# Kernel tuning notes

Measured on AMD Instinct MI355X. Metric: run time of the kernel, lower is better.

## Reference

```python
import jax, jax.numpy as jnp
import numpy as np

B, NQ, NKV = 2, 2048, 2048
DIM, CTX_DIM = 1024, 1024
HEADS, DIM_HEAD = 16, 64
INNER = HEADS * DIM_HEAD  # 1024
SCALE = DIM_HEAD ** -0.5


def setup_inputs() -> dict:
    key = jax.random.key(0)
    ks = jax.random.split(key, 6)
    x = jax.random.normal(ks[0], (B, NQ, DIM), dtype=jnp.float32)
    context = jax.random.normal(ks[1], (B, NKV, CTX_DIM), dtype=jnp.float32)
    # nn.Linear weights stored as [out, in] in torch; we keep [in, out] for x @ W.
    Wq = jax.random.normal(ks[2], (DIM, INNER), dtype=jnp.float32) / np.sqrt(DIM)
    Wkv = jax.random.normal(ks[3], (CTX_DIM, 2 * INNER), dtype=jnp.float32) / np.sqrt(CTX_DIM)
    Wout = jax.random.normal(ks[4], (INNER, DIM), dtype=jnp.float32) / np.sqrt(INNER)
    bout = jax.random.normal(ks[5], (DIM,), dtype=jnp.float32) * 0.01
    return {"x": x, "context": context, "Wq": Wq, "Wkv": Wkv, "Wout": Wout, "bout": bout}


def reference(x, context, Wq, Wkv, Wout, bout):
    q = x @ Wq                      # [B, Nq, inner]
    kv = context @ Wkv              # [B, Nkv, 2*inner]
    k, v = jnp.split(kv, 2, axis=-1)

    def split_heads(t):             # [B, N, inner] -> [B, H, N, dh]
        return t.reshape(t.shape[0], t.shape[1], HEADS, DIM_HEAD).transpose(0, 2, 1, 3)

    q, k, v = split_heads(q), split_heads(k), split_heads(v)
    dots = jnp.einsum('bhqd,bhkd->bhqk', q, k) * SCALE  # [B, H, Nq, Nkv]
    attn = jax.nn.softmax(dots, axis=-1)
    out = jnp.einsum('bhqk,bhkd->bhqd', attn, v)        # [B, H, Nq, dh]
    out = out.transpose(0, 2, 1, 3).reshape(out.shape[0], out.shape[2], INNER)
    return out @ Wout + bout        # [B, Nq, dim]
```

## Files before the change

### kernel.cpp

```cpp
#include <hip/hip_runtime.h>
#include <hip/hip_bf16.h>
#include <stdint.h>

#define NQ 2048
#define NKV 2048
#define DIM 1024
#define INNER 1024
#define HEADS 16
#define DH 64
#define BATCH 2

typedef float f32x4 __attribute__((ext_vector_type(4)));
typedef __bf16 bf16x8 __attribute__((ext_vector_type(8)));
typedef unsigned int u32x4 __attribute__((ext_vector_type(4)));

__device__ inline ushort f2b(float f) {
    uint32_t u = __builtin_bit_cast(uint32_t, f);
    u += 0x7fff + ((u >> 16) & 1);
    return (ushort)(u >> 16);
}

__device__ inline uint pkbf16(float lo, float hi) {
    __hip_bfloat162 h = __float22bfloat162_rn(make_float2(lo, hi));
    uint r;
    __builtin_memcpy(&r, &h, 4);
    return r;
}

__device__ __forceinline__ void gload16(const void* g, void* lds) {
    __builtin_amdgcn_global_load_lds(
        (const __attribute__((address_space(1))) unsigned int*)g,
        (__attribute__((address_space(3))) unsigned int*)lds, 16, 0, 0);
}

__global__ void cvt2(const float* __restrict__ a, ushort* __restrict__ oa,
                     const float* __restrict__ b, ushort* __restrict__ ob, int n4) {
    int i = blockIdx.x * blockDim.x + threadIdx.x;
    int stride = gridDim.x * blockDim.x;
    for (; i < 2 * n4; i += stride) {
        float4 v;
        if (i < n4) v = ((const float4*)a)[i];
        else        v = ((const float4*)b)[i - n4];
        ushort4 o;
        o.x = f2b(v.x); o.y = f2b(v.y); o.z = f2b(v.z); o.w = f2b(v.w);
        if (i < n4) ((ushort4*)oa)[i] = o;
        else        ((ushort4*)ob)[i - n4] = o;
    }
}

__global__ void transp4(const float* __restrict__ Wq, const float* __restrict__ Wkv,
                        const float* __restrict__ Wout,
                        ushort* __restrict__ Wqt, ushort* __restrict__ Wkvt,
                        ushort* __restrict__ Woutt) {
    __shared__ ushort tile[32][33];
    int z = blockIdx.z;
    const float* src; ushort* dst; int C;
    if (z == 0)      { src = Wq;          dst = Wqt;                C = 1024; }
    else if (z == 1) { src = Wkv;         dst = Wkvt;               C = 2048; }
    else if (z == 2) { src = Wkv + 1024;  dst = Wkvt + 1024 * 1024; C = 2048; }
    else             { src = Wout;        dst = Woutt;              C = 1024; }
    int c0 = blockIdx.x * 32, r0 = blockIdx.y * 32;
    int tx = threadIdx.x, ty = threadIdx.y;
#pragma unroll
    for (int i = 0; i < 4; i++)
        tile[ty + i * 8][tx] = f2b(src[(size_t)(r0 + ty + i * 8) * C + c0 + tx]);
    __syncthreads();
#pragma unroll
    for (int i = 0; i < 4; i++)
        dst[(size_t)(c0 + ty + i * 8) * 1024 + r0 + tx] = tile[tx][ty + i * 8];
}

__global__ __launch_bounds__(256) void vtransp(const ushort* __restrict__ vb, ushort* __restrict__ vtb) {
    __shared__ ushort tile[64][72];
    int kt = blockIdx.x, h = blockIdx.y, b = blockIdx.z;
    int t = threadIdx.x;
    const ushort* src = vb + ((size_t)b * NKV + kt * 64) * INNER + h * DH;
#pragma unroll
    for (int p = 0; p < 2; p++) {
        int kv = p * 32 + (t >> 3), c0 = (t & 7) * 8;
        u32x4 v = *(const u32x4*)&src[(size_t)kv * INNER + c0];
        *(u32x4*)&tile[kv][c0] = v;
    }
    __syncthreads();
    ushort* dst = vtb + (((size_t)b * HEADS + h) * DH) * NKV + kt * 64;
#pragma unroll
    for (int p = 0; p < 2; p++) {
        int d = p * 32 + (t >> 3), k0 = (t & 7) * 8;
        ushort tmp[8];
#pragma unroll
        for (int j = 0; j < 8; j++) tmp[j] = tile[k0 + j][d];
        *(u32x4*)&dst[(size_t)d * NKV + k0] = *(u32x4*)tmp;
    }
}

template <int MODE, int BN>
__global__ __launch_bounds__(256) void gemm_bt(const ushort* __restrict__ A, const ushort* __restrict__ Bt,
                                               void* __restrict__ C0, void* __restrict__ C1,
                                               const float* __restrict__ bias, float oscale,
                                               int M, int N, int K) {
    constexpr int NI = BN / 32;
    constexpr int NL = (BN == 128) ? 4 : 3;
    __shared__ ushort As[2][4096];
    __shared__ ushort Bs[2][BN * 32];
    int m0 = blockIdx.y * 128, n0 = blockIdx.x * BN;
    int t = threadIdx.x, l = t & 63, w = t >> 6;
    int wr = w >> 1, wc = w & 1;
    int lg = l >> 4, lc = l & 15;
    f32x4 acc[4][NI] = {};

    auto stage = [&](int buf, int k0) {
#pragma unroll
        for (int i = 0; i < 2; i++) {
            int s = w + i * 4;
            gload16(A + (size_t)(m0 + (s & 1) * 64 + l) * K + k0 + (s >> 1) * 8, &As[buf][s * 512]);
        }
        if (BN == 128) {
#pragma unroll
            for (int i = 0; i < 2; i++) {
                int s = w + i * 4;
                gload16(Bt + (size_t)(n0 + (s & 1) * 64 + l) * K + k0 + (s >> 1) * 8, &Bs[buf][s * 512]);
            }
        } else {
            gload16(Bt + (size_t)(n0 + l) * K + k0 + w * 8, &Bs[buf][w * 512]);
        }
    };

    stage(0, 0);
    for (int k0 = 0, tt = 0; k0 < K; k0 += 32, ++tt) {
        int cur = tt & 1;
        if (k0 + 32 < K) {
            stage(cur ^ 1, k0 + 32);
            asm volatile("s_waitcnt vmcnt(%0)" :: "n"(NL) : "memory");
        } else {
            asm volatile("s_waitcnt vmcnt(0)" ::: "memory");
        }
        __builtin_amdgcn_s_barrier();
        asm volatile("" ::: "memory");
        bf16x8 af[4], bf[NI];
#pragma unroll
        for (int mi = 0; mi < 4; mi++)
            af[mi] = *(const bf16x8*)&As[cur][(lg * 128 + wr * 64 + mi * 16 + lc) * 8];
#pragma unroll
        for (int ni = 0; ni < NI; ni++)
            bf[ni] = *(const bf16x8*)&Bs[cur][(lg * BN + wc * (BN / 2) + ni * 16 + lc) * 8];
        __builtin_amdgcn_s_setprio(1);
#pragma unroll
        for (int mi = 0; mi < 4; mi++)
#pragma unroll
            for (int ni = 0; ni < NI; ni++)
                acc[mi][ni] = __builtin_amdgcn_mfma_f32_16x16x32_bf16(af[mi], bf[ni], acc[mi][ni], 0, 0, 0);
        __builtin_amdgcn_s_setprio(0);
        asm volatile("s_waitcnt lgkmcnt(0)" ::: "memory");
        __builtin_amdgcn_s_barrier();
        asm volatile("" ::: "memory");
    }
#pragma unroll
    for (int mi = 0; mi < 4; mi++)
#pragma unroll
        for (int ni = 0; ni < NI; ni++)
#pragma unroll
            for (int r = 0; r < 4; r++) {
                int m = m0 + wr * 64 + mi * 16 + lg * 4 + r;
                int n = n0 + wc * (BN / 2) + ni * 16 + lc;
                float v = acc[mi][ni][r];
                if (MODE == 0) {
                    ((ushort*)C0)[(size_t)m * N + n] = f2b(v * oscale);
                } else if (MODE == 1) {
                    if (n < 1024) ((ushort*)C0)[(size_t)m * 1024 + n] = f2b(v);
                    else          ((ushort*)C1)[(size_t)m * 1024 + (n - 1024)] = f2b(v);
                } else {
                    ((float*)C0)[(size_t)m * N + n] = v + bias[n];
                }
            }
}

__global__ __launch_bounds__(128, 2) void attn3(const ushort* __restrict__ qb, const ushort* __restrict__ kb,
                                                const ushort* __restrict__ vtb, ushort* __restrict__ ob) {
    __shared__ ushort Qs[8 * 64 * 8];
    __shared__ ushort Ks[2][4096];
    __shared__ ushort Vs[2][4096];
    int flat = blockIdx.x;
    int swz = (flat & 7) * 128 + (flat >> 3);
    int qt = swz & 31, h = (swz >> 5) & 15, b = swz >> 9;
    int t = threadIdx.x, l = t & 63, w = t >> 6;
    int lg = l >> 4, lc = l & 15;
    int xsw = (lc << 1) & 0x1C;
    const ushort* Qg = qb + (size_t)b * NQ * INNER + h * DH;
    const ushort* Kg = kb + (size_t)b * NKV * INNER + h * DH;
    const ushort* Vg = vtb + (((size_t)b * HEADS + h) * DH) * NKV;
    int q0 = qt * 64;

#pragma unroll
    for (int i = 0; i < 4; i++) {
        int s = w * 4 + i;
        gload16(Qg + (size_t)(q0 + l) * INNER + s * 8, &Qs[s * 512]);
    }
    auto stageKV = [&](int buf, int kv0) {
#pragma unroll
        for (int i = 0; i < 4; i++) {
            int s = w * 4 + i;
            gload16(Kg + (size_t)(kv0 + l) * INNER + s * 8, &Ks[buf][s * 512]);
            gload16(Vg + (size_t)l * NKV + kv0 + s * 8, &Vs[buf][s * 512]);
        }
    };
    stageKV(0, 0);
    __syncthreads();

    bf16x8 qf[2][2];
#pragma unroll
    for (int mi = 0; mi < 2; mi++)
#pragma unroll
        for (int kc = 0; kc < 2; kc++)
            qf[mi][kc] = *(const bf16x8*)&Qs[((kc * 4 + lg) * 64 + w * 32 + mi * 16 + lc) * 8];
    __syncthreads();

    uint* Ps = (uint*)Qs + w * 1024;
    f32x4 o[2][4] = {};
    float m_[2] = {-1e30f, -1e30f}, s_[2] = {0.f, 0.f};

    for (int tt = 0; tt < NKV / 64; ++tt) {
        int cur = tt & 1;
        if (tt + 1 < NKV / 64) stageKV(cur ^ 1, (tt + 1) * 64);
        f32x4 st[2][4] = {};
        __builtin_amdgcn_s_setprio(1);
#pragma unroll
        for (int kc = 0; kc < 2; kc++)
#pragma unroll
            for (int nb = 0; nb < 4; nb++) {
                bf16x8 kf = *(const bf16x8*)&Ks[cur][((kc * 4 + lg) * 64 + nb * 16 + lc) * 8];
                st[0][nb] = __builtin_amdgcn_mfma_f32_16x16x32_bf16(kf, qf[0][kc], st[0][nb], 0, 0, 0);
                st[1][nb] = __builtin_amdgcn_mfma_f32_16x16x32_bf16(kf, qf[1][kc], st[1][nb], 0, 0, 0);
            }
        __builtin_amdgcn_s_setprio(0);
#pragma unroll
        for (int mi = 0; mi < 2; mi++) {
            float mx = st[mi][0][0];
#pragma unroll
            for (int nb = 0; nb < 4; nb++)
#pragma unroll
                for (int r = 0; r < 4; r++) mx = fmaxf(mx, st[mi][nb][r]);
            mx = fmaxf(mx, __shfl_xor(mx, 16));
            mx = fmaxf(mx, __shfl_xor(mx, 32));
            float mn = fmaxf(m_[mi], mx);
            float fac = __builtin_amdgcn_exp2f(m_[mi] - mn);
            m_[mi] = mn;
            s_[mi] *= fac;
#pragma unroll
            for (int nb = 0; nb < 4; nb++) o[mi][nb] *= fac;
            float rs = 0.f;
#pragma unroll
            for (int nb = 0; nb < 4; nb++) {
                float p0 = __builtin_amdgcn_exp2f(st[mi][nb][0] - mn);
                float p1 = __builtin_amdgcn_exp2f(st[mi][nb][1] - mn);
                float p2 = __builtin_amdgcn_exp2f(st[mi][nb][2] - mn);
                float p3 = __builtin_amdgcn_exp2f(st[mi][nb][3] - mn);
                rs += (p0 + p1) + (p2 + p3);
                uint2 pw;
                pw.x = pkbf16(p0, p1);
                pw.y = pkbf16(p2, p3);
                *(uint2*)&Ps[(mi * 16 + lc) * 32 + ((nb * 8 + lg * 2) ^ xsw)] = pw;
            }
            rs += __shfl_xor(rs, 16);
            rs += __shfl_xor(rs, 32);
            s_[mi] += rs;
        }
        asm volatile("" ::: "memory");
        bf16x8 pf[2][2], vf[4][2];
#pragma unroll
        for (int mi = 0; mi < 2; mi++)
#pragma unroll
            for (int kc = 0; kc < 2; kc++)
                pf[mi][kc] = *(const bf16x8*)&Ps[(mi * 16 + lc) * 32 + ((kc * 16 + lg * 4) ^ xsw)];
#pragma unroll
        for (int nb = 0; nb < 4; nb++)
#pragma unroll
            for (int kc = 0; kc < 2; kc++)
                vf[nb][kc] = *(const bf16x8*)&Vs[cur][((kc * 4 + lg) * 64 + nb * 16 + lc) * 8];
        __builtin_amdgcn_s_setprio(1);
#pragma unroll
        for (int nb = 0; nb < 4; nb++)
#pragma unroll
            for (int kc = 0; kc < 2; kc++) {
                o[0][nb] = __builtin_amdgcn_mfma_f32_16x16x32_bf16(vf[nb][kc], pf[0][kc], o[0][nb], 0, 0, 0);
                o[1][nb] = __builtin_amdgcn_mfma_f32_16x16x32_bf16(vf[nb][kc], pf[1][kc], o[1][nb], 0, 0, 0);
            }
        __builtin_amdgcn_s_setprio(0);
        __syncthreads();
    }
    ushort* Og = ob + (size_t)b * NQ * INNER + h * DH;
#pragma unroll
    for (int mi = 0; mi < 2; mi++) {
        float inv = 1.f / s_[mi];
        int q = q0 + w * 32 + mi * 16 + lc;
#pragma unroll
        for (int nb = 0; nb < 4; nb++) {
            uint2 pw;
            pw.x = pkbf16(o[mi][nb][0] * inv, o[mi][nb][1] * inv);
            pw.y = pkbf16(o[mi][nb][2] * inv, o[mi][nb][3] * inv);
            *(uint2*)&Og[(size_t)q * INNER + nb * 16 + lg * 4] = pw;
        }
    }
}

extern "C" void kernel_launch(void* const* d_in, const int* in_sizes, int n_in,
                              void* d_out, int out_size, void* d_ws, size_t ws_size,
                              hipStream_t stream) {
    const float* x    = (const float*)d_in[0];
    const float* ctx  = (const float*)d_in[1];
    const float* Wq   = (const float*)d_in[2];
    const float* Wkv  = (const float*)d_in[3];
    const float* Wout = (const float*)d_in[4];
    const float* bout = (const float*)d_in[5];
    float* out = (float*)d_out;

    if (ws_size < (size_t)(56u << 20)) return;
    char* ws = (char*)d_ws;
    ushort* xb    = (ushort*)(ws);
    ushort* vtb   = (ushort*)(ws);
    ushort* cb    = (ushort*)(ws + (8u << 20));
    ushort* ob    = (ushort*)(ws + (8u << 20));
    ushort* qb    = (ushort*)(ws + (16u << 20));
    ushort* kb    = (ushort*)(ws + (24u << 20));
    ushort* vb    = (ushort*)(ws + (32u << 20));
    ushort* Wqt   = (ushort*)(ws + (48u << 20));
    ushort* Wkvt  = (ushort*)(ws + (50u << 20));
    ushort* Woutt = (ushort*)(ws + (54u << 20));

    cvt2<<<2048, 256, 0, stream>>>(x, xb, ctx, cb, (BATCH * NQ * DIM) / 4);
    transp4<<<dim3(32, 32, 4), dim3(32, 8), 0, stream>>>(Wq, Wkv, Wout, Wqt, Wkvt, Woutt);

    gemm_bt<0, 64><<<dim3(16, 32), 256, 0, stream>>>(xb, Wqt, qb, nullptr, nullptr, 0.125f * 1.44269504f, 4096, 1024, 1024);
    gemm_bt<1, 128><<<dim3(16, 32), 256, 0, stream>>>(cb, Wkvt, kb, vb, nullptr, 1.f, 4096, 2048, 1024);
    vtransp<<<dim3(32, 16, 2), 256, 0, stream>>>(vb, vtb);
    attn3<<<1024, 128, 0, stream>>>(qb, kb, vtb, ob);
    gemm_bt<2, 64><<<dim3(16, 32), 256, 0, stream>>>(ob, Woutt, out, nullptr, bout, 1.f, 4096, 1024, 1024);
}
```

Before: 197.3 us.

## Fuse prep kernels, merge QKV GEMMs with V-transpose epilogue, enlarge attention tiles

Merges the input conversion and weight transposes into one prep launch. The Q and KV projections run in a single GEMM launch, and the V transpose is folded into the GEMM epilogue, which removes the separate vtransp kernel and its round trip through memory. The attention kernel moves to 256-thread blocks with 128-row Q tiles and skips the online-softmax rescale when the running max grows by at most 8. The lazy rescale can lose a little precision, and the changed occupancy and LDS footprint of the attention kernel may shift its performance either way.

```diff
diff --git a/kernel.cpp b/kernel.cpp
--- a/kernel.cpp
+++ b/kernel.cpp
@@ -33,95 +33,69 @@
         (__attribute__((address_space(3))) unsigned int*)lds, 16, 0, 0);
 }
 
-__global__ void cvt2(const float* __restrict__ a, ushort* __restrict__ oa,
-                     const float* __restrict__ b, ushort* __restrict__ ob, int n4) {
-    int i = blockIdx.x * blockDim.x + threadIdx.x;
-    int stride = gridDim.x * blockDim.x;
-    for (; i < 2 * n4; i += stride) {
-        float4 v;
-        if (i < n4) v = ((const float4*)a)[i];
-        else        v = ((const float4*)b)[i - n4];
-        ushort4 o;
-        o.x = f2b(v.x); o.y = f2b(v.y); o.z = f2b(v.z); o.w = f2b(v.w);
-        if (i < n4) ((ushort4*)oa)[i] = o;
-        else        ((ushort4*)ob)[i - n4] = o;
-    }
-}
-
-__global__ void transp4(const float* __restrict__ Wq, const float* __restrict__ Wkv,
-                        const float* __restrict__ Wout,
-                        ushort* __restrict__ Wqt, ushort* __restrict__ Wkvt,
-                        ushort* __restrict__ Woutt) {
-    __shared__ ushort tile[32][33];
+__global__ void prep(const float* __restrict__ x, const float* __restrict__ ctx,
+                     const float* __restrict__ Wq, const float* __restrict__ Wkv,
+                     const float* __restrict__ Wout,
+                     ushort* __restrict__ xb, ushort* __restrict__ cb,
+                     ushort* __restrict__ Wqt, ushort* __restrict__ Wkvt,
+                     ushort* __restrict__ Woutt) {
     int z = blockIdx.z;
-    const float* src; ushort* dst; int C;
-    if (z == 0)      { src = Wq;          dst = Wqt;                C = 1024; }
-    else if (z == 1) { src = Wkv;         dst = Wkvt;               C = 2048; }
-    else if (z == 2) { src = Wkv + 1024;  dst = Wkvt + 1024 * 1024; C = 2048; }
-    else             { src = Wout;        dst = Woutt;              C = 1024; }
-    int c0 = blockIdx.x * 32, r0 = blockIdx.y * 32;
-    int tx = threadIdx.x, ty = threadIdx.y;
-#pragma unroll
-    for (int i = 0; i < 4; i++)
-        tile[ty + i * 8][tx] = f2b(src[(size_t)(r0 + ty + i * 8) * C + c0 + tx]);
-    __syncthreads();
-#pragma unroll
-    for (int i = 0; i < 4; i++)
-        dst[(size_t)(c0 + ty + i * 8) * 1024 + r0 + tx] = tile[tx][ty + i * 8];
-}
-
-__global__ __launch_bounds__(256) void vtransp(const ushort* __restrict__ vb, ushort* __restrict__ vtb) {
-    __shared__ ushort tile[64][72];
-    int kt = blockIdx.x, h = blockIdx.y, b = blockIdx.z;
-    int t = threadIdx.x;
-    const ushort* src = vb + ((size_t)b * NKV + kt * 64) * INNER + h * DH;
-#pragma unroll
-    for (int p = 0; p < 2; p++) {
-        int kv = p * 32 + (t >> 3), c0 = (t & 7) * 8;
-        u32x4 v = *(const u32x4*)&src[(size_t)kv * INNER + c0];
-        *(u32x4*)&tile[kv][c0] = v;
-    }
-    __syncthreads();
-    ushort* dst = vtb + (((size_t)b * HEADS + h) * DH) * NKV + kt * 64;
-#pragma unroll
-    for (int p = 0; p < 2; p++) {
-        int d = p * 32 + (t >> 3), k0 = (t & 7) * 8;
-        ushort tmp[8];
-#pragma unroll
-        for (int j = 0; j < 8; j++) tmp[j] = tile[k0 + j][d];
-        *(u32x4*)&dst[(size_t)d * NKV + k0] = *(u32x4*)tmp;
-    }
-}
-
-template <int MODE, int BN>
-__global__ __launch_bounds__(256) void gemm_bt(const ushort* __restrict__ A, const ushort* __restrict__ Bt,
-                                               void* __restrict__ C0, void* __restrict__ C1,
-                                               const float* __restrict__ bias, float oscale,
-                                               int M, int N, int K) {
-    constexpr int NI = BN / 32;
-    constexpr int NL = (BN == 128) ? 4 : 3;
+    if (z < 4) {
+        __shared__ ushort tile[32][33];
+        const float* src; ushort* dst; int C;
+        if (z == 0)      { src = Wq;          dst = Wqt;                C = 1024; }
+        else if (z == 1) { src = Wkv;         dst = Wkvt;               C = 2048; }
+        else if (z == 2) { src = Wkv + 1024;  dst = Wkvt + 1024 * 1024; C = 2048; }
+        else             { src = Wout;        dst = Woutt;              C = 1024; }
+        int c0 = blockIdx.x * 32, r0 = blockIdx.y * 32;
+        int tx = threadIdx.x, ty = threadIdx.y;
+#pragma unroll
+        for (int i = 0; i < 4; i++)
+            tile[ty + i * 8][tx] = f2b(src[(size_t)(r0 + ty + i * 8) * C + c0 + tx]);
+        __syncthreads();
+#pragma unroll
+        for (int i = 0; i < 4; i++)
+            dst[(size_t)(c0 + ty + i * 8) * 1024 + r0 + tx] = tile[tx][ty + i * 8];
+    } else {
+        const int n4 = (BATCH * NQ * DIM) / 4;
+        int fb = blockIdx.y * 32 + blockIdx.x;
+        int t = threadIdx.y * 32 + threadIdx.x;
+        for (int i = fb * 256 + t; i < 2 * n4; i += 1024 * 256) {
+            float4 v;
+            if (i < n4) v = ((const float4*)x)[i];
+            else        v = ((const float4*)ctx)[i - n4];
+            ushort4 o;
+            o.x = f2b(v.x); o.y = f2b(v.y); o.z = f2b(v.z); o.w = f2b(v.w);
+            if (i < n4) ((ushort4*)xb)[i] = o;
+            else        ((ushort4*)cb)[i - n4] = o;
+        }
+    }
+}
+
+__global__ __launch_bounds__(256) void gemm_qkv(const ushort* __restrict__ xb, const ushort* __restrict__ cb,
+                                                const ushort* __restrict__ Wqt, const ushort* __restrict__ Wkvt,
+                                                ushort* __restrict__ qb, ushort* __restrict__ kb,
+                                                ushort* __restrict__ vtb, float qscale) {
+    constexpr int K = 1024;
     __shared__ ushort As[2][4096];
-    __shared__ ushort Bs[2][BN * 32];
-    int m0 = blockIdx.y * 128, n0 = blockIdx.x * BN;
+    __shared__ ushort Bs[2][4096];
+    int bid = blockIdx.x;
+    bool isq = bid < 256;
+    const ushort *A, *Bt;
+    int m0, n0;
+    if (isq) { A = xb; Bt = Wqt;  m0 = (bid >> 3) * 128; n0 = (bid & 7) * 128; }
+    else     { int b2 = bid - 256; A = cb; Bt = Wkvt; m0 = (b2 >> 4) * 128; n0 = (b2 & 15) * 128; }
     int t = threadIdx.x, l = t & 63, w = t >> 6;
     int wr = w >> 1, wc = w & 1;
     int lg = l >> 4, lc = l & 15;
-    f32x4 acc[4][NI] = {};
+    f32x4 acc[4][4] = {};
 
     auto stage = [&](int buf, int k0) {
 #pragma unroll
         for (int i = 0; i < 2; i++) {
             int s = w + i * 4;
             gload16(A + (size_t)(m0 + (s & 1) * 64 + l) * K + k0 + (s >> 1) * 8, &As[buf][s * 512]);
-        }
-        if (BN == 128) {
-#pragma unroll
-            for (int i = 0; i < 2; i++) {
-                int s = w + i * 4;
-                gload16(Bt + (size_t)(n0 + (s & 1) * 64 + l) * K + k0 + (s >> 1) * 8, &Bs[buf][s * 512]);
-            }
-        } else {
-            gload16(Bt + (size_t)(n0 + l) * K + k0 + w * 8, &Bs[buf][w * 512]);
+            gload16(Bt + (size_t)(n0 + (s & 1) * 64 + l) * K + k0 + (s >> 1) * 8, &Bs[buf][s * 512]);
         }
     };
 
@@ -130,75 +104,155 @@
         int cur = tt & 1;
         if (k0 + 32 < K) {
             stage(cur ^ 1, k0 + 32);
-            asm volatile("s_waitcnt vmcnt(%0)" :: "n"(NL) : "memory");
+            asm volatile("s_waitcnt vmcnt(4)" ::: "memory");
         } else {
             asm volatile("s_waitcnt vmcnt(0)" ::: "memory");
         }
         __builtin_amdgcn_s_barrier();
         asm volatile("" ::: "memory");
-        bf16x8 af[4], bf[NI];
+        bf16x8 af[4], bf[4];
 #pragma unroll
         for (int mi = 0; mi < 4; mi++)
             af[mi] = *(const bf16x8*)&As[cur][(lg * 128 + wr * 64 + mi * 16 + lc) * 8];
 #pragma unroll
-        for (int ni = 0; ni < NI; ni++)
-            bf[ni] = *(const bf16x8*)&Bs[cur][(lg * BN + wc * (BN / 2) + ni * 16 + lc) * 8];
+        for (int ni = 0; ni < 4; ni++)
+            bf[ni] = *(const bf16x8*)&Bs[cur][(lg * 128 + wc * 64 + ni * 16 + lc) * 8];
         __builtin_amdgcn_s_setprio(1);
 #pragma unroll
         for (int mi = 0; mi < 4; mi++)
 #pragma unroll
-            for (int ni = 0; ni < NI; ni++)
+            for (int ni = 0; ni < 4; ni++)
                 acc[mi][ni] = __builtin_amdgcn_mfma_f32_16x16x32_bf16(af[mi], bf[ni], acc[mi][ni], 0, 0, 0);
         __builtin_amdgcn_s_setprio(0);
         asm volatile("s_waitcnt lgkmcnt(0)" ::: "memory");
         __builtin_amdgcn_s_barrier();
         asm volatile("" ::: "memory");
     }
+    if (isq) {
+#pragma unroll
+        for (int mi = 0; mi < 4; mi++)
+#pragma unroll
+            for (int ni = 0; ni < 4; ni++)
+#pragma unroll
+                for (int r = 0; r < 4; r++) {
+                    int m = m0 + wr * 64 + mi * 16 + lg * 4 + r;
+                    int n = n0 + wc * 64 + ni * 16 + lc;
+                    qb[(size_t)m * 1024 + n] = f2b(acc[mi][ni][r] * qscale);
+                }
+    } else if (n0 < 1024) {
+#pragma unroll
+        for (int mi = 0; mi < 4; mi++)
+#pragma unroll
+            for (int ni = 0; ni < 4; ni++)
+#pragma unroll
+                for (int r = 0; r < 4; r++) {
+                    int m = m0 + wr * 64 + mi * 16 + lg * 4 + r;
+                    int n = n0 + wc * 64 + ni * 16 + lc;
+                    kb[(size_t)m * 1024 + n] = f2b(acc[mi][ni][r]);
+                }
+    } else {
+#pragma unroll
+        for (int mi = 0; mi < 4; mi++)
+#pragma unroll
+            for (int ni = 0; ni < 4; ni++) {
+                int n = n0 - 1024 + wc * 64 + ni * 16 + lc;
+                int h = n >> 6, d = n & 63;
+                int mrow = m0 + wr * 64 + mi * 16 + lg * 4;
+                int b = mrow >> 11, kv = mrow & 2047;
+                ushort4 pk;
+                pk.x = f2b(acc[mi][ni][0]); pk.y = f2b(acc[mi][ni][1]);
+                pk.z = f2b(acc[mi][ni][2]); pk.w = f2b(acc[mi][ni][3]);
+                *(ushort4*)&vtb[(((size_t)b * HEADS + h) * DH + d) * (size_t)NKV + kv] = pk;
+            }
+    }
+}
+
+__global__ __launch_bounds__(256) void gemm_out(const ushort* __restrict__ A, const ushort* __restrict__ Bt,
+                                                float* __restrict__ C0, const float* __restrict__ bias,
+                                                int M, int N, int K) {
+    __shared__ ushort As[2][4096];
+    __shared__ ushort Bs[2][2048];
+    int m0 = blockIdx.y * 128, n0 = blockIdx.x * 64;
+    int t = threadIdx.x, l = t & 63, w = t >> 6;
+    int wr = w >> 1, wc = w & 1;
+    int lg = l >> 4, lc = l & 15;
+    f32x4 acc[4][2] = {};
+
+    auto stage = [&](int buf, int k0) {
+#pragma unroll
+        for (int i = 0; i < 2; i++) {
+            int s = w + i * 4;
+            gload16(A + (size_t)(m0 + (s & 1) * 64 + l) * K + k0 + (s >> 1) * 8, &As[buf][s * 512]);
+        }
+        gload16(Bt + (size_t)(n0 + l) * K + k0 + w * 8, &Bs[buf][w * 512]);
+    };
+
+    stage(0, 0);
+    for (int k0 = 0, tt = 0; k0 < K; k0 += 32, ++tt) {
+        int cur = tt & 1;
+        if (k0 + 32 < K) {
+            stage(cur ^ 1, k0 + 32);
+            asm volatile("s_waitcnt vmcnt(3)" ::: "memory");
+        } else {
+            asm volatile("s_waitcnt vmcnt(0)" ::: "memory");
+        }
+        __builtin_amdgcn_s_barrier();
+        asm volatile("" ::: "memory");
+        bf16x8 af[4], bf[2];
+#pragma unroll
+        for (int mi = 0; mi < 4; mi++)
+            af[mi] = *(const bf16x8*)&As[cur][(lg * 128 + wr * 64 + mi * 16 + lc) * 8];
+#pragma unroll
+        for (int ni = 0; ni < 2; ni++)
+            bf[ni] = *(const bf16x8*)&Bs[cur][(lg * 64 + wc * 32 + ni * 16 + lc) * 8];
+        __builtin_amdgcn_s_setprio(1);
+#pragma unroll
+        for (int mi = 0; mi < 4; mi++)
+#pragma unroll
+            for (int ni = 0; ni < 2; ni++)
+                acc[mi][ni] = __builtin_amdgcn_mfma_f32_16x16x32_bf16(af[mi], bf[ni], acc[mi][ni], 0, 0, 0);
+        __builtin_amdgcn_s_setprio(0);
+        asm volatile("s_waitcnt lgkmcnt(0)" ::: "memory");
+        __builtin_amdgcn_s_barrier();
+        asm volatile("" ::: "memory");
+    }
 #pragma unroll
     for (int mi = 0; mi < 4; mi++)
 #pragma unroll
-        for (int ni = 0; ni < NI; ni++)
+        for (int ni = 0; ni < 2; ni++)
 #pragma unroll
             for (int r = 0; r < 4; r++) {
                 int m = m0 + wr * 64 + mi * 16 + lg * 4 + r;
-                int n = n0 + wc * (BN / 2) + ni * 16 + lc;
-                float v = acc[mi][ni][r];
-                if (MODE == 0) {
-                    ((ushort*)C0)[(size_t)m * N + n] = f2b(v * oscale);
-                } else if (MODE == 1) {
-                    if (n < 1024) ((ushort*)C0)[(size_t)m * 1024 + n] = f2b(v);
-                    else          ((ushort*)C1)[(size_t)m * 1024 + (n - 1024)] = f2b(v);
-                } else {
-                    ((float*)C0)[(size_t)m * N + n] = v + bias[n];
-                }
-            }
-}
-
-__global__ __launch_bounds__(128, 2) void attn3(const ushort* __restrict__ qb, const ushort* __restrict__ kb,
+                int n = n0 + wc * 32 + ni * 16 + lc;
+                C0[(size_t)m * N + n] = acc[mi][ni][r] + bias[n];
+            }
+}
+
+__global__ __launch_bounds__(256, 3) void attn3(const ushort* __restrict__ qb, const ushort* __restrict__ kb,
                                                 const ushort* __restrict__ vtb, ushort* __restrict__ ob) {
-    __shared__ ushort Qs[8 * 64 * 8];
+    __shared__ ushort Qs[8 * 128 * 8];
     __shared__ ushort Ks[2][4096];
     __shared__ ushort Vs[2][4096];
     int flat = blockIdx.x;
-    int swz = (flat & 7) * 128 + (flat >> 3);
-    int qt = swz & 31, h = (swz >> 5) & 15, b = swz >> 9;
+    int swz = (flat & 7) * 64 + (flat >> 3);
+    int qt = swz & 15, h = (swz >> 4) & 15, b = swz >> 8;
     int t = threadIdx.x, l = t & 63, w = t >> 6;
     int lg = l >> 4, lc = l & 15;
     int xsw = (lc << 1) & 0x1C;
     const ushort* Qg = qb + (size_t)b * NQ * INNER + h * DH;
     const ushort* Kg = kb + (size_t)b * NKV * INNER + h * DH;
     const ushort* Vg = vtb + (((size_t)b * HEADS + h) * DH) * NKV;
-    int q0 = qt * 64;
+    int q0 = qt * 128;
 
 #pragma unroll
     for (int i = 0; i < 4; i++) {
         int s = w * 4 + i;
-        gload16(Qg + (size_t)(q0 + l) * INNER + s * 8, &Qs[s * 512]);
+        gload16(Qg + (size_t)(q0 + (s & 1) * 64 + l) * INNER + (s >> 1) * 8, &Qs[s * 512]);
     }
     auto stageKV = [&](int buf, int kv0) {
 #pragma unroll
-        for (int i = 0; i < 4; i++) {
-            int s = w * 4 + i;
+        for (int i = 0; i < 2; i++) {
+            int s = w + i * 4;
             gload16(Kg + (size_t)(kv0 + l) * INNER + s * 8, &Ks[buf][s * 512]);
             gload16(Vg + (size_t)l * NKV + kv0 + s * 8, &Vs[buf][s * 512]);
         }
@@ -211,7 +265,7 @@
     for (int mi = 0; mi < 2; mi++)
 #pragma unroll
         for (int kc = 0; kc < 2; kc++)
-            qf[mi][kc] = *(const bf16x8*)&Qs[((kc * 4 + lg) * 64 + w * 32 + mi * 16 + lc) * 8];
+            qf[mi][kc] = *(const bf16x8*)&Qs[((kc * 4 + lg) * 128 + w * 32 + mi * 16 + lc) * 8];
     __syncthreads();
 
     uint* Ps = (uint*)Qs + w * 1024;
@@ -241,12 +295,15 @@
                 for (int r = 0; r < 4; r++) mx = fmaxf(mx, st[mi][nb][r]);
             mx = fmaxf(mx, __shfl_xor(mx, 16));
             mx = fmaxf(mx, __shfl_xor(mx, 32));
-            float mn = fmaxf(m_[mi], mx);
-            float fac = __builtin_amdgcn_exp2f(m_[mi] - mn);
-            m_[mi] = mn;
-            s_[mi] *= fac;
-#pragma unroll
-            for (int nb = 0; nb < 4; nb++) o[mi][nb] *= fac;
+            if (!__all(mx - m_[mi] <= 8.f)) {
+                float mn = fmaxf(m_[mi], mx);
+                float fac = __builtin_amdgcn_exp2f(m_[mi] - mn);
+                m_[mi] = mn;
+                s_[mi] *= fac;
+#pragma unroll
+                for (int nb = 0; nb < 4; nb++) o[mi][nb] *= fac;
+            }
+            float mn = m_[mi];
             float rs = 0.f;
 #pragma unroll
             for (int nb = 0; nb < 4; nb++) {
@@ -316,22 +373,17 @@
     if (ws_size < (size_t)(56u << 20)) return;
     char* ws = (char*)d_ws;
     ushort* xb    = (ushort*)(ws);
-    ushort* vtb   = (ushort*)(ws);
     ushort* cb    = (ushort*)(ws + (8u << 20));
     ushort* ob    = (ushort*)(ws + (8u << 20));
     ushort* qb    = (ushort*)(ws + (16u << 20));
     ushort* kb    = (ushort*)(ws + (24u << 20));
-    ushort* vb    = (ushort*)(ws + (32u << 20));
+    ushort* vtb   = (ushort*)(ws + (32u << 20));
     ushort* Wqt   = (ushort*)(ws + (48u << 20));
     ushort* Wkvt  = (ushort*)(ws + (50u << 20));
     ushort* Woutt = (ushort*)(ws + (54u << 20));
 
-    cvt2<<<2048, 256, 0, stream>>>(x, xb, ctx, cb, (BATCH * NQ * DIM) / 4);
-    transp4<<<dim3(32, 32, 4), dim3(32, 8), 0, stream>>>(Wq, Wkv, Wout, Wqt, Wkvt, Woutt);
-
-    gemm_bt<0, 64><<<dim3(16, 32), 256, 0, stream>>>(xb, Wqt, qb, nullptr, nullptr, 0.125f * 1.44269504f, 4096, 1024, 1024);
-    gemm_bt<1, 128><<<dim3(16, 32), 256, 0, stream>>>(cb, Wkvt, kb, vb, nullptr, 1.f, 4096, 2048, 1024);
-    vtransp<<<dim3(32, 16, 2), 256, 0, stream>>>(vb, vtb);
-    attn3<<<1024, 128, 0, stream>>>(qb, kb, vtb, ob);
-    gemm_bt<2, 64><<<dim3(16, 32), 256, 0, stream>>>(ob, Woutt, out, nullptr, bout, 1.f, 4096, 1024, 1024);
-}
+    prep<<<dim3(32, 32, 5), dim3(32, 8), 0, stream>>>(x, ctx, Wq, Wkv, Wout, xb, cb, Wqt, Wkvt, Woutt);
+    gemm_qkv<<<768, 256, 0, stream>>>(xb, cb, Wqt, Wkvt, qb, kb, vtb, 0.125f * 1.44269504f);
+    attn3<<<512, 256, 0, stream>>>(qb, kb, vtb, ob);
+    gemm_out<<<dim3(16, 32), 256, 0, stream>>>(ob, Woutt, out, bout, 4096, 1024, 1024);
+}
```

New measurement: 193.1 us. 2.2% less time.
